# Optimization experiments

Hardware: AMD Instinct MI355X
Metric: run time of the kernel (lower is better)

## Reference

```python
import jax, jax.numpy as jnp
import numpy as np
import math

D_MODEL = 512
EXPAND = 2
D_INNER = EXPAND * D_MODEL          # 1024
HEADDIM = 8
NHEADS = D_INNER // HEADDIM         # 128
NGROUPS = 2
D_STATE = 16
CONV_DIM = D_INNER + 2 * NGROUPS * D_STATE   # 1088
D_IN_PROJ = 2 * D_INNER + 2 * NGROUPS * D_STATE + NHEADS  # 2240
P13 = [(0, 0), (1, 1)]
P31 = [(1, 1), (0, 0)]
P33 = [(1, 1), (1, 1)]


def silu(x):
    return x * jax.nn.sigmoid(x)


def dwconv(x, w, pad):
    # depthwise 2D conv; x: (B,C,H,W), w: (C,1,kh,kw)
    return jax.lax.conv_general_dilated(
        x, w, (1, 1), pad,
        dimension_numbers=('NCHW', 'OIHW', 'NCHW'),
        feature_group_count=x.shape[1])


def interleave_ch(a, b):
    # channel-interleave: out[:, ::2] = a, out[:, 1::2] = b
    Bn, C, Hh, Ww = a.shape
    return jnp.stack([a, b], axis=2).reshape(Bn, 2 * C, Hh, Ww)


def linear_attn(x, dt, A, Bm, Cm, Dp):
    # non-causal linear-attention duality of Mamba2 (grouped heads)
    # x: (B,L,h,p), dt: (B,L,h), A: (h,) negative, Bm/Cm: (B,L,g*ds), Dp: (h,)
    b, L, h, p = x.shape
    g, ds = NGROUPS, D_STATE
    dA = -(dt * A[None, None, :])          # ssd_positive_dA -> positive
    Vs = x * dA[..., None]
    K = Bm.reshape(b, L, g, ds)
    Q = Cm.reshape(b, L, g, ds)
    Vg = Vs.reshape(b, L, h // g, g, p)
    KV = jnp.einsum('blgs,blmgp->bmgsp', K, Vg)       # (b, h/g, g, ds, p)
    y = jnp.einsum('blgs,bmgsp->blmgp', Q, KV)        # (b, L, h/g, g, p)
    y = y + (x * Dp[None, None, :, None]).reshape(b, L, h // g, g, p)
    return y.reshape(b, L, h, p)


def setup_inputs() -> dict:
    key = jax.random.key(0)
    ks = jax.random.split(key, 20)
    Bn, Hh, Ww = 8, 64, 64
    L = Hh * Ww
    u = jax.random.normal(ks[0], (Bn, L, D_MODEL), jnp.float32)
    W_in = jax.random.normal(ks[1], (D_IN_PROJ, D_MODEL), jnp.float32) / math.sqrt(D_MODEL)
    dt = jnp.exp(jax.random.uniform(ks[2], (NHEADS,)) * (math.log(0.1) - math.log(0.001)) + math.log(0.001))
    dt = jnp.clip(dt, 1e-4, None)
    dt_bias = dt + jnp.log(-jnp.expm1(-dt))
    A_log = jnp.log(jax.random.uniform(ks[3], (NHEADS,), minval=1.0, maxval=16.0))
    Dp = jnp.ones((NHEADS,), jnp.float32)

    def cw(k, c, kh, kw):
        return jax.random.normal(k, (c, 1, kh, kw), jnp.float32) / math.sqrt(kh * kw)

    bcC = 2 * NGROUPS * D_STATE // 4  # 16
    w_conv2d = cw(ks[4], CONV_DIM // 2, 3, 3)
    w13x1 = cw(ks[5], D_INNER // 4, 1, 3)
    w31x1 = cw(ks[6], D_INNER // 4, 3, 1)
    w13x2 = cw(ks[7], D_INNER // 4, 1, 3)
    w31x2 = cw(ks[8], D_INNER // 4, 3, 1)
    w13bc1 = cw(ks[9], bcC, 1, 3)
    w31bc1 = cw(ks[10], bcC, 3, 1)
    w13bc2 = cw(ks[11], bcC, 1, 3)
    w31bc2 = cw(ks[12], bcC, 3, 1)
    w_conv2d_z = cw(ks[13], D_INNER, 3, 3)
    ln_g = jnp.ones((D_INNER,), jnp.float32)
    ln_b = jnp.zeros((D_INNER,), jnp.float32)
    scale = jnp.float32(1.0)
    shift = jnp.float32(0.0)
    alpha1 = jnp.float32(1.0)
    alpha2 = jnp.float32(1.0)
    W_out = jax.random.normal(ks[14], (D_MODEL, 2 * D_INNER), jnp.float32) / math.sqrt(2 * D_INNER)
    return dict(u=u, H=Hh, W=Ww, W_in=W_in, dt_bias=dt_bias, A_log=A_log, Dp=Dp,
                w_conv2d=w_conv2d, w13x1=w13x1, w31x1=w31x1, w13x2=w13x2, w31x2=w31x2,
                w13bc1=w13bc1, w31bc1=w31bc1, w13bc2=w13bc2, w31bc2=w31bc2,
                w_conv2d_z=w_conv2d_z, ln_g=ln_g, ln_b=ln_b, scale=scale, shift=shift,
                alpha1=alpha1, alpha2=alpha2, W_out=W_out)


def reference(u, H, W, W_in, dt_bias, A_log, Dp, w_conv2d, w13x1, w31x1, w13x2, w31x2,
              w13bc1, w31bc1, w13bc2, w31bc2, w_conv2d_z, ln_g, ln_b, scale, shift,
              alpha1, alpha2, W_out):
    Bn, L, _ = u.shape
    zxbcdt = u @ W_in.T                                 # (B,L,2240)
    z = zxbcdt[..., :D_INNER]
    xBC = zxbcdt[..., D_INNER:D_INNER + CONV_DIM]
    dt = zxbcdt[..., D_INNER + CONV_DIM:]
    dt = jax.nn.softplus(dt + dt_bias)                  # (B,L,h)

    # even/odd channel-interleave split, reshape to NCHW feature maps
    even = xBC[..., 0::2].reshape(Bn, H, W, -1).transpose(0, 3, 1, 2)
    odd = xBC[..., 1::2].reshape(Bn, H, W, -1).transpose(0, 3, 1, 2)
    even = silu(dwconv(even, w_conv2d, P33))

    oe = odd[:, 0::2]
    oo = odd[:, 1::2]
    x_oe, bc_oe = oe[:, :D_INNER // 4], oe[:, D_INNER // 4:]
    x_oo, bc_oo = oo[:, :D_INNER // 4], oo[:, D_INNER // 4:]
    x_oe = silu(dwconv(dwconv(x_oe, w31x1, P31), w13x1, P13))
    x_oo = silu(dwconv(dwconv(x_oo, w13x2, P13), w31x2, P31))
    bc_oe = silu(dwconv(dwconv(bc_oe, w13bc1, P13), w31bc1, P31))
    bc_oo = silu(dwconv(dwconv(bc_oo, w31bc2, P31), w13bc2, P13))
    xbc_oe = jnp.concatenate([x_oe, bc_oe], axis=1)
    xbc_oo = jnp.concatenate([x_oo, bc_oo], axis=1)
    odd = interleave_ch(xbc_oe, xbc_oo)

    xBCc = interleave_ch(even, odd)                     # (B, CONV_DIM, H, W)
    xBCc = xBCc.transpose(0, 2, 3, 1).reshape(Bn, L, CONV_DIM)
    x = xBCc[..., :D_INNER]
    Bm = xBCc[..., D_INNER:D_INNER + NGROUPS * D_STATE]
    Cm = xBCc[..., D_INNER + NGROUPS * D_STATE:]

    A = -jnp.exp(A_log)
    y = linear_attn(x.reshape(Bn, L, NHEADS, HEADDIM), dt, A, Bm, Cm, Dp)
    y = y.reshape(Bn, L, D_INNER)

    mu = y.mean(-1, keepdims=True)
    var = ((y - mu) ** 2).mean(-1, keepdims=True)
    y = (y - mu) / jnp.sqrt(var + 1e-5) * ln_g + ln_b
    y = y * scale + shift

    zc = z.reshape(Bn, H, W, D_INNER).transpose(0, 3, 1, 2)
    zc = silu(dwconv(zc, w_conv2d_z, P33))
    zc = zc.transpose(0, 2, 3, 1).reshape(Bn, L, D_INNER)

    out = jnp.concatenate([alpha1 * y, alpha2 * zc], axis=-1) @ W_out.T
    return out
```

## Files before the change

### kernel.cpp

```cpp
#include <hip/hip_runtime.h>
#include <hip/hip_bf16.h>
#include <cstdint>
#include <cstddef>

#define HDIM    64
#define WDIM    64
#define LPB     4096
#define DMODEL  512
#define DIN     1024
#define CONVD   1088
#define DPROJ   2240
#define NHEADS  128
#define NCV     2112

using f16    = _Float16;
using f16x4  = __attribute__((ext_vector_type(4))) _Float16;
using f16x8  = __attribute__((ext_vector_type(8))) _Float16;
using f32x4  = __attribute__((ext_vector_type(4))) float;

__device__ __forceinline__ float siluf(float x) { return x / (1.f + __expf(-x)); }
__device__ __forceinline__ float fsilu(float x) {
  return x * __builtin_amdgcn_rcpf(1.f + __expf(-x));
}

__device__ __forceinline__ void fma_mix_lo(float& acc, unsigned a, unsigned b) {
  asm("v_fma_mix_f32 %0, %1, %2, %0 op_sel_hi:[1,1,0]" : "+v"(acc) : "v"(a), "v"(b));
}
__device__ __forceinline__ void fma_mix_hi(float& acc, unsigned a, unsigned b) {
  asm("v_fma_mix_f32 %0, %1, %2, %0 op_sel:[1,1,0] op_sel_hi:[1,1,0]" : "+v"(acc) : "v"(a), "v"(b));
}
__device__ __forceinline__ void fmixl(float& acc, unsigned a, float b) {
  asm("v_fma_mix_f32 %0, %1, %2, %0 op_sel_hi:[1,0,0]" : "+v"(acc) : "v"(a), "v"(b));
}
__device__ __forceinline__ void fmixh(float& acc, unsigned a, float b) {
  asm("v_fma_mix_f32 %0, %1, %2, %0 op_sel:[1,0,0] op_sel_hi:[1,0,0]" : "+v"(acc) : "v"(a), "v"(b));
}

__device__ __forceinline__ void fma8(float* acc, const uint4& v, const uint4& w) {
  fma_mix_lo(acc[0], v.x, w.x);  fma_mix_hi(acc[1], v.x, w.x);
  fma_mix_lo(acc[2], v.y, w.y);  fma_mix_hi(acc[3], v.y, w.y);
  fma_mix_lo(acc[4], v.z, w.z);  fma_mix_hi(acc[5], v.z, w.z);
  fma_mix_lo(acc[6], v.w, w.w);  fma_mix_hi(acc[7], v.w, w.w);
}

__global__ __launch_bounds__(256) void k_cvt(const float* __restrict__ in, f16* __restrict__ out) {
  size_t i = ((size_t)blockIdx.x * 256 + threadIdx.x) * 4;
  f32x4 v = *(const f32x4*)(in + i);
  f16x4 o;
  #pragma unroll
  for (int j = 0; j < 4; ++j) o[j] = (f16)v[j];
  *(f16x4*)(out + i) = o;
}

__global__ __launch_bounds__(256) void k_cvt_win(const float* __restrict__ W, f16* __restrict__ out) {
  int i = blockIdx.x * 256 + threadIdx.x;
  int row = i >> 9, col = i & 511;
  float v = (row < DPROJ) ? W[row * 512 + col] : 0.f;
  out[i] = (f16)v;
}

__global__ __launch_bounds__(256) void k_keff(const float* __restrict__ w33,
                       const float* __restrict__ w13x1, const float* __restrict__ w31x1,
                       const float* __restrict__ w13x2, const float* __restrict__ w31x2,
                       const float* __restrict__ w13bc1, const float* __restrict__ w31bc1,
                       const float* __restrict__ w13bc2, const float* __restrict__ w31bc2,
                       const float* __restrict__ wz,
                       f16* __restrict__ keffall) {
  int j = blockIdx.x * 256 + threadIdx.x;
  if (j >= NCV) return;
  if (j < 1024) {
    #pragma unroll
    for (int tap = 0; tap < 9; ++tap) keffall[tap * NCV + j] = (f16)wz[j * 9 + tap];
    return;
  }
  int jj = j - 1024;
  float kh[3] = {0,0,0}, kw[3] = {0,0,0};
  bool dense = ((jj & 1) == 0);
  if (!dense) {
    int m = jj >> 2;
    if ((jj & 3) == 1) {
      if (m < 256) { for (int t=0;t<3;++t){ kh[t]=w31x1[m*3+t];  kw[t]=w13x1[m*3+t];  } }
      else { int q=m-256; for (int t=0;t<3;++t){ kh[t]=w31bc1[q*3+t]; kw[t]=w13bc1[q*3+t]; } }
    } else {
      if (m < 256) { for (int t=0;t<3;++t){ kh[t]=w31x2[m*3+t];  kw[t]=w13x2[m*3+t];  } }
      else { int q=m-256; for (int t=0;t<3;++t){ kh[t]=w31bc2[q*3+t]; kw[t]=w13bc2[q*3+t]; } }
    }
  }
  #pragma unroll
  for (int dh = 0; dh < 3; ++dh)
    #pragma unroll
    for (int dw = 0; dw < 3; ++dw) {
      float v = dense ? w33[(jj >> 1) * 9 + dh*3 + dw] : kh[dh] * kw[dw];
      keffall[(dh*3 + dw) * NCV + j] = (f16)v;
    }
}

template<typename OutT>
__global__ __launch_bounds__(256) void k_gemmf(const f16* __restrict__ A, int lda,
                                               const f16* __restrict__ Bm, int ldb,
                                               OutT* __restrict__ C, int ldc,
                                               int Kseg, int NW, int ntn, int ntmn, long Cseg) {
  __shared__ __align__(16) f16 As[128 * 32];
  __shared__ __align__(16) f16 Bs[128 * 32];

  int nwg = gridDim.x, bid = blockIdx.x;
  int q = nwg >> 3, r = nwg & 7;
  int xcd = bid & 7, loc = bid >> 3;
  int wg  = (xcd < r ? xcd * (q + 1) : r * (q + 1) + (xcd - r) * q) + loc;
  int kseg = wg / ntmn;
  int rem  = wg - kseg * ntmn;
  long m0 = (long)(rem / ntn) * 128;
  long n0 = (long)(rem % ntn) * 128;
  const int kbase = kseg * Kseg;

  const int tid  = threadIdx.x;
  const int w    = tid >> 6, lane = tid & 63;
  const int wr   = w >> 1, wc = w & 1;

  f32x4 acc[4][4];
  #pragma unroll
  for (int i = 0; i < 4; ++i)
    #pragma unroll
    for (int j = 0; j < 4; ++j) acc[i][j] = (f32x4){0.f,0.f,0.f,0.f};

  const int srow = w * 16 + (lane >> 2);
  const int scol = (lane & 3) * 8;
  const long aoff = (m0 + srow) * (long)lda + scol + kbase;
  const long boff = (n0 + srow) * (long)ldb + scol + kbase;
  const int fr = lane & 15;
  const int kc = (lane >> 4) * 8;

  for (int k0 = 0; k0 < Kseg; k0 += 32) {
    #pragma unroll
    for (int i = 0; i < 2; ++i) {
      long ao = aoff + (long)i*64*lda + k0;
      long bo = boff + (long)i*64*ldb + k0;
      int ls = (i*4 + w) * 512;
      __builtin_amdgcn_global_load_lds((const __attribute__((address_space(1))) void*)(A + ao),
                                       (__attribute__((address_space(3))) void*)&As[ls], 16, 0, 0);
      __builtin_amdgcn_global_load_lds((const __attribute__((address_space(1))) void*)(Bm + bo),
                                       (__attribute__((address_space(3))) void*)&Bs[ls], 16, 0, 0);
    }
    __syncthreads();
    f16x8 af[4], bf[4];
    #pragma unroll
    for (int f = 0; f < 4; ++f) {
      af[f] = *(const f16x8*)&As[(wr*64 + f*16 + fr) * 32 + kc];
      bf[f] = *(const f16x8*)&Bs[(wc*64 + f*16 + fr) * 32 + kc];
    }
    #pragma unroll
    for (int i = 0; i < 4; ++i)
      #pragma unroll
      for (int j = 0; j < 4; ++j)
        acc[i][j] = __builtin_amdgcn_mfma_f32_16x16x32_f16(af[i], bf[j], acc[i][j], 0, 0, 0);
    __syncthreads();
  }

  OutT* Cb = C + (long)kseg * Cseg;
  const int cr = (lane >> 4) * 4;
  const int cc = lane & 15;
  #pragma unroll
  for (int i = 0; i < 4; ++i) {
    long rbase = m0 + wr*64 + i*16 + cr;
    #pragma unroll
    for (int j = 0; j < 4; ++j) {
      int col = (int)n0 + wc*64 + j*16 + cc;
      if (col < NW) {
        OutT* cp = Cb + rbase * (long)ldc + col;
        #pragma unroll
        for (int r = 0; r < 4; ++r) cp[(long)r * ldc] = (OutT)acc[i][j][r];
      }
    }
  }
}

__global__ __launch_bounds__(256) void k_red2h(const f16* __restrict__ part, long seg,
                                               float* __restrict__ out) {
  long i = ((long)blockIdx.x * 256 + threadIdx.x) * 4;
  f16x4 s0 = *(const f16x4*)(part + i);
  f16x4 s1 = *(const f16x4*)(part + seg + i);
  f32x4 o;
  #pragma unroll
  for (int j = 0; j < 4; ++j) o[j] = (float)s0[j] + (float)s1[j];
  *(f32x4*)(out + i) = o;
}

__global__ __launch_bounds__(192) void k_conv_all(const f16* __restrict__ zx,
                                                  const f16* __restrict__ keffall,
                                                  const float* __restrict__ a2_p,
                                                  const float* __restrict__ dt_bias,
                                                  const float* __restrict__ A_log,
                                                  f16* __restrict__ xbc,
                                                  f16* __restrict__ g2,
                                                  float* __restrict__ dAb) {
  int t = threadIdx.x;
  int bid = blockIdx.x, qq = gridDim.x >> 3;
  int grp = (bid & 7) * qq + (bid >> 3);
  int l0 = grp * 2;
  long lb = (long)(l0 & ~(LPB - 1));
  int h  = (l0 >> 6) & 63;
  int w0 = l0 & 63;

  if (t < 132) {
    int c0 = t * 8;
    int c1 = c0 + 1056;
    float a00[8] = {0,0,0,0,0,0,0,0};
    float a01[8] = {0,0,0,0,0,0,0,0};
    float a10[8] = {0,0,0,0,0,0,0,0};
    float a11[8] = {0,0,0,0,0,0,0,0};
    const uint4 z4 = {0u,0u,0u,0u};

    #pragma unroll
    for (int dh = 0; dh < 3; ++dh) {
      int hh = h + dh - 1;
      if (hh < 0 || hh >= HDIM) continue;
      const f16* rp = zx + (lb + (long)(hh * 64)) * DPROJ;
      uint4 v0[4], v1[4];
      #pragma unroll
      for (int pp = 0; pp < 4; ++pp) {
        int ww = w0 + pp - 1;
        ww = ww < 0 ? 0 : (ww > 63 ? 63 : ww);
        const f16* tp = rp + (long)ww * DPROJ;
        v0[pp] = *(const uint4*)(tp + c0);
        v1[pp] = *(const uint4*)(tp + c1);
      }
      if (w0 == 0)  { v0[0] = z4; v1[0] = z4; }
      if (w0 == 62) { v0[3] = z4; v1[3] = z4; }
      #pragma unroll
      for (int dw = 0; dw < 3; ++dw) {
        uint4 wa = *(const uint4*)&keffall[(dh*3 + dw) * NCV + c0];
        uint4 wb = *(const uint4*)&keffall[(dh*3 + dw) * NCV + c1];
        fma8(a00, v0[dw],     wa);
        fma8(a10, v0[dw + 1], wa);
        fma8(a01, v1[dw],     wb);
        fma8(a11, v1[dw + 1], wb);
      }
    }

    float a2 = a2_p[0];
    #pragma unroll
    for (int ti = 0; ti < 2; ++ti) {
      long l = l0 + ti;
      const float* pc0 = ti ? a10 : a00;
      const float* pc1 = ti ? a11 : a01;
      f16x8 o8;
      if (c0 < 1024) {
        #pragma unroll
        for (int j = 0; j < 8; ++j) o8[j] = (f16)(a2 * fsilu(pc0[j]));
        *(f16x8*)&g2[l * 2048 + 1024 + c0] = o8;
      } else {
        #pragma unroll
        for (int j = 0; j < 8; ++j) o8[j] = (f16)fsilu(pc0[j]);
        *(f16x8*)&xbc[l * (long)CONVD + (c0 - 1024)] = o8;
      }
      f16x8 o9;
      #pragma unroll
      for (int j = 0; j < 8; ++j) o9[j] = (f16)fsilu(pc1[j]);
      *(f16x8*)&xbc[l * (long)CONVD + (c1 - 1024)] = o9;
    }
  } else if (t < 164) {
    int idx = t - 132;
    int ti = idx >> 4;
    int hd = (idx & 15) * 8;
    long l = l0 + ti;
    f16x8 x = *(const f16x8*)&zx[l * (long)DPROJ + NCV + hd];
    f32x4 o0, o1;
    #pragma unroll
    for (int j = 0; j < 8; ++j) {
      float xx = (float)x[j] + dt_bias[hd + j];
      float sp = (xx > 20.f) ? xx : log1pf(__expf(xx));
      float dv = sp * __expf(A_log[hd + j]);
      if (j < 4) o0[j] = dv; else o1[j-4] = dv;
    }
    *(f32x4*)&dAb[l * 128 + hd]     = o0;
    *(f32x4*)&dAb[l * 128 + hd + 4] = o1;
  }
}

__global__ __launch_bounds__(512) void k_kv_part(const f16* __restrict__ xbc,
                                                 const float* __restrict__ dA,
                                                 float* __restrict__ part) {
  int t = threadIdx.x;
  int m = t >> 3, p = t & 7;
  int lc = blockIdx.x, b = blockIdx.y;
  float acc0[16], acc1[16];
  #pragma unroll
  for (int s = 0; s < 16; ++s) { acc0[s] = 0.f; acc1[s] = 0.f; }
  long lbase = (long)b * LPB + lc * 32;
  #pragma unroll 2
  for (int li = 0; li < 32; ++li) {
    long row = lbase + li;
    const f16* xr = xbc + row * CONVD;
    float2 aa = *(const float2*)&dA[row * 128 + 2*m];
    float xv0 = (float)xr[16*m + p]     * aa.x;
    float xv1 = (float)xr[16*m + 8 + p] * aa.y;
    uint4 q0 = *(const uint4*)(xr + DIN);
    uint4 q1 = *(const uint4*)(xr + DIN + 8);
    uint4 q2 = *(const uint4*)(xr + DIN + 16);
    uint4 q3 = *(const uint4*)(xr + DIN + 24);
    unsigned a0[4] = {q0.x, q0.y, q0.z, q0.w};
    unsigned a1[4] = {q1.x, q1.y, q1.z, q1.w};
    unsigned a2v[4] = {q2.x, q2.y, q2.z, q2.w};
    unsigned a3[4] = {q3.x, q3.y, q3.z, q3.w};
    #pragma unroll
    for (int k = 0; k < 4; ++k) {
      fmixl(acc0[2*k],     a0[k], xv0);  fmixh(acc0[2*k+1],     a0[k], xv0);
      fmixl(acc0[8+2*k],   a1[k], xv0);  fmixh(acc0[8+2*k+1],   a1[k], xv0);
      fmixl(acc1[2*k],     a2v[k], xv1); fmixh(acc1[2*k+1],     a2v[k], xv1);
      fmixl(acc1[8+2*k],   a3[k], xv1);  fmixh(acc1[8+2*k+1],   a3[k], xv1);
    }
  }
  long base = ((long)(b*128 + lc)) * 16384 + (long)m * 256;
  #pragma unroll
  for (int s = 0; s < 16; ++s) {
    part[base + s*8 + p]       = acc0[s];
    part[base + 128 + s*8 + p] = acc1[s];
  }
}

__global__ __launch_bounds__(256) void k_kv_red(const float* __restrict__ part,
                                                float* __restrict__ KV) {
  int e = blockIdx.x * 256 + threadIdx.x;
  int b = blockIdx.y;
  float s = 0.f;
  #pragma unroll 4
  for (int lc = 0; lc < 128; ++lc) s += part[((long)(b*128 + lc)) * 16384 + e];
  KV[(long)b * 16384 + e] = s;
}

__global__ __launch_bounds__(256) void k_y_ln(const f16* __restrict__ xbc,
                                              const float* __restrict__ KV,
                                              const float* __restrict__ Dp,
                                              const float* __restrict__ ln_g,
                                              const float* __restrict__ ln_b,
                                              const float* __restrict__ sc_p,
                                              const float* __restrict__ sh_p,
                                              const float* __restrict__ a1_p,
                                              f16* __restrict__ g2) {
  __shared__ float Qs[32][32];
  __shared__ float red[2][8];
  int t = threadIdx.x;
  int hd = t >> 1, pb = (t & 1) * 4;
  int m = hd >> 1, g = hd & 1;
  int b = blockIdx.x >> 7;
  long l0 = (long)b * LPB + (blockIdx.x & 127) * 32;

  f32x4 kv[16];
  #pragma unroll
  for (int s = 0; s < 16; ++s)
    kv[s] = *(const f32x4*)&KV[(long)b * 16384 + m*256 + g*128 + s*8 + pb];

  if (t < 128) {
    int tok = t >> 2, q8 = (t & 3) * 8;
    f16x8 qv = *(const f16x8*)&xbc[(l0 + tok) * CONVD + 1056 + q8];
    #pragma unroll
    for (int j = 0; j < 8; ++j) Qs[tok][q8 + j] = (float)qv[j];
  }
  int c0 = hd*8 + pb;
  f32x4 lg = *(const f32x4*)&ln_g[c0];
  f32x4 lb = *(const f32x4*)&ln_b[c0];
  float dpv = Dp[hd];
  float sc = sc_p[0], sh = sh_p[0], a1 = a1_p[0];
  int wv = t >> 6, lane = t & 63;
  __syncthreads();

  for (int tok = 0; tok < 32; ++tok) {
    long row = l0 + tok;
    f16x4 xr4 = *(const f16x4*)&xbc[row * CONVD + c0];
    f32x4 yv;
    #pragma unroll
    for (int j = 0; j < 4; ++j) yv[j] = (float)xr4[j] * dpv;
    #pragma unroll
    for (int s = 0; s < 16; ++s) {
      float qv = Qs[tok][g*16 + s];
      #pragma unroll
      for (int j = 0; j < 4; ++j) yv[j] = fmaf(qv, kv[s][j], yv[j]);
    }
    float s1 = yv[0] + yv[1] + yv[2] + yv[3];
    float s2 = yv[0]*yv[0] + yv[1]*yv[1] + yv[2]*yv[2] + yv[3]*yv[3];
    #pragma unroll
    for (int off = 1; off < 64; off <<= 1) {
      s1 += __shfl_xor(s1, off, 64);
      s2 += __shfl_xor(s2, off, 64);
    }
    if (lane == 0) { red[tok & 1][wv*2] = s1; red[tok & 1][wv*2 + 1] = s2; }
    __syncthreads();
    const float* rr = red[tok & 1];
    float S1 = rr[0] + rr[2] + rr[4] + rr[6];
    float S2 = rr[1] + rr[3] + rr[5] + rr[7];
    float mu   = S1 * (1.f/1024.f);
    float var  = S2 * (1.f/1024.f) - mu*mu;
    float rstd = rsqrtf(var + 1e-5f);
    f16x4 o4;
    #pragma unroll
    for (int j = 0; j < 4; ++j) {
      float yn = (yv[j] - mu) * rstd * lg[j] + lb[j];
      o4[j] = (f16)(a1 * (yn * sc + sh));
    }
    *(f16x4*)&g2[row * 2048 + c0] = o4;
  }
}

extern "C" void kernel_launch(void* const* d_in, const int* in_sizes, int n_in,
                              void* d_out, int out_size, void* d_ws, size_t ws_size,
                              hipStream_t stream) {
  const float* u       = (const float*)d_in[0];
  const float* W_in    = (const float*)d_in[3];
  const float* dt_bias = (const float*)d_in[4];
  const float* A_log   = (const float*)d_in[5];
  const float* Dp      = (const float*)d_in[6];
  const float* w33     = (const float*)d_in[7];
  const float* w13x1   = (const float*)d_in[8];
  const float* w31x1   = (const float*)d_in[9];
  const float* w13x2   = (const float*)d_in[10];
  const float* w31x2   = (const float*)d_in[11];
  const float* w13bc1  = (const float*)d_in[12];
  const float* w31bc1  = (const float*)d_in[13];
  const float* w13bc2  = (const float*)d_in[14];
  const float* w31bc2  = (const float*)d_in[15];
  const float* wz      = (const float*)d_in[16];
  const float* ln_g    = (const float*)d_in[17];
  const float* ln_b    = (const float*)d_in[18];
  const float* sc      = (const float*)d_in[19];
  const float* sh      = (const float*)d_in[20];
  const float* a1      = (const float*)d_in[21];
  const float* a2      = (const float*)d_in[22];
  const float* W_out   = (const float*)d_in[23];

  const size_t B_G2   = 16777216;
  const size_t B_ZX   = 18350080;
  const size_t B_XBC  = 8912896;
  const size_t B_DA   = 2097152;
  const size_t B_KV   = 65536;
  const size_t perC   = B_G2 + B_ZX + B_XBC + B_DA + B_KV;
  const size_t persist = 2359296 + 2097152 + 38912;

  int C = 8;
  while (C > 1 && persist + (size_t)C * perC > ws_size) C >>= 1;
  const int nch = 8 / C;
  const int Mc  = C * LPB;

  char* p = (char*)d_ws;
  f16*   win_f   = (f16*)p;   p += 2359296;
  f16*   wout_f  = (f16*)p;   p += 2097152;
  f16*   keffall = (f16*)p;   p += 38912;
  char*  arena   = p;
  f16*   g2      = (f16*)arena;
  f16*   u_f     = (f16*)arena;
  p = arena + (size_t)C * B_G2;
  f16*   zx      = (f16*)p;   p += (size_t)C * B_ZX;
  f16*   xbc     = (f16*)p;   p += (size_t)C * B_XBC;
  float* dAb     = (float*)p; p += (size_t)C * B_DA;
  float* KV      = (float*)p; p += (size_t)C * B_KV;
  float* part   = (float*)zx;
  f16*   kpart  = (f16*)zx;

  k_cvt_win<<<4608, 256, 0, stream>>>(W_in, win_f);
  k_cvt    <<<1024, 256, 0, stream>>>(W_out, wout_f);
  k_keff   <<<9, 256, 0, stream>>>(w33, w13x1, w31x1, w13x2, w31x2,
                                   w13bc1, w31bc1, w13bc2, w31bc2, wz, keffall);

  for (int ch = 0; ch < nch; ++ch) {
    const float* uc   = u + (size_t)ch * Mc * 512;
    float*       outc = (float*)d_out + (size_t)ch * Mc * 512;
    const int ntm = Mc / 128;

    k_cvt<<<Mc/2, 256, 0, stream>>>(uc, u_f);

    k_gemmf<f16><<<ntm*18, 256, 0, stream>>>(u_f, 512, win_f, 512,
                                             zx, DPROJ, 512, DPROJ, 18, ntm*18, 0);

    k_conv_all<<<Mc/2, 192, 0, stream>>>(zx, keffall, a2, dt_bias, A_log,
                                         xbc, g2, dAb);

    k_kv_part <<<dim3(128, C), 512, 0, stream>>>(xbc, dAb, part);
    k_kv_red  <<<dim3(64, C), 256, 0, stream>>>(part, KV);
    k_y_ln    <<<C*128, 256, 0, stream>>>(xbc, KV, Dp, ln_g, ln_b, sc, sh, a1, g2);

    const long cseg = (long)Mc * 512;
    k_gemmf<f16><<<ntm*4*2, 256, 0, stream>>>(g2, 2048, wout_f, 2048,
                                              kpart, 512, 1024, 512, 4, ntm*4, cseg);
    k_red2h<<<Mc/2, 256, 0, stream>>>(kpart, cseg, outc);
  }
}
```

Measured before the change: 539.7 us.

## Use 256x256-tile double-buffered GEMM with direct-to-LDS loads for input projection

Adds a new GEMM kernel for the input projection with 256x256 output tiles, 512 threads and one workgroup per CU. It double-buffers 64-wide K slices in LDS using global_load_lds, with XOR swizzling and staged vmcnt waits so the next tile's loads overlap the current tile's MFMAs. The larger tile is meant to raise data reuse and cut global traffic, and the explicit pipeline aims to hide memory latency. In exchange it uses far more registers and LDS, launches fewer workgroups, and relies on hand-counted waitcnts for correctness.

```diff
diff --git a/kernel.cpp b/kernel.cpp
--- a/kernel.cpp
+++ b/kernel.cpp
@@ -18,6 +18,9 @@
 using f16x8  = __attribute__((ext_vector_type(8))) _Float16;
 using f32x4  = __attribute__((ext_vector_type(4))) float;
 
+#define VM_CNT(n) asm volatile("s_waitcnt vmcnt(" #n ")" ::: "memory")
+#define LDSFENCE  asm volatile("" ::: "memory")
+
 __device__ __forceinline__ float siluf(float x) { return x / (1.f + __expf(-x)); }
 __device__ __forceinline__ float fsilu(float x) {
   return x * __builtin_amdgcn_rcpf(1.f + __expf(-x));
@@ -35,7 +38,6 @@
 __device__ __forceinline__ void fmixh(float& acc, unsigned a, float b) {
   asm("v_fma_mix_f32 %0, %1, %2, %0 op_sel:[1,0,0] op_sel_hi:[1,0,0]" : "+v"(acc) : "v"(a), "v"(b));
 }
-
 __device__ __forceinline__ void fma8(float* acc, const uint4& v, const uint4& w) {
   fma_mix_lo(acc[0], v.x, w.x);  fma_mix_hi(acc[1], v.x, w.x);
   fma_mix_lo(acc[2], v.y, w.y);  fma_mix_hi(acc[3], v.y, w.y);
@@ -95,6 +97,133 @@
     }
 }
 
+__global__ __launch_bounds__(512, 1) void k_gemm8(const f16* __restrict__ A, int lda,
+                                                  const f16* __restrict__ Bm, int ldb,
+                                                  f16* __restrict__ C, int ldc,
+                                                  int K, int NW, int ntn) {
+  __shared__ __align__(16) f16 Al[2 * 16384];
+  __shared__ __align__(16) f16 Bl[2 * 16384];
+
+  int nwg = gridDim.x, bid = blockIdx.x;
+  int q = nwg >> 3, r = nwg & 7;
+  int xcd = bid & 7, loc = bid >> 3;
+  int wg  = (xcd < r ? xcd * (q + 1) : r * (q + 1) + (xcd - r) * q) + loc;
+  long m0 = (long)(wg / ntn) * 256;
+  long n0 = (long)(wg % ntn) * 256;
+
+  const int tid  = threadIdx.x;
+  const int wid  = tid >> 6, lane = tid & 63;
+  const int wr   = wid >> 2, wc = wid & 3;
+
+  const int rowoff = wid * 8 + (lane >> 3);
+  const int scolS  = ((lane & 7) ^ (lane >> 3)) * 8;
+  const int ldst   = wid * 512;
+
+  const int fr   = lane & 15;
+  const int koff = (lane >> 4) * 8;
+  const int swz8 = (lane & 7) << 3;
+
+  f32x4 acc[8][4];
+  #pragma unroll
+  for (int i = 0; i < 8; ++i)
+    #pragma unroll
+    for (int j = 0; j < 4; ++j) acc[i][j] = (f32x4){0.f,0.f,0.f,0.f};
+
+  const int NT = K >> 6;
+
+  auto stA = [&](int par, int X, int kb) {
+    __builtin_amdgcn_global_load_lds(
+      (const __attribute__((address_space(1))) void*)(A + (m0 + X*64 + rowoff) * (long)lda + kb + scolS),
+      (__attribute__((address_space(3))) void*)&Al[par*16384 + X*4096 + ldst], 16, 0, 0);
+  };
+  auto stB = [&](int par, int X, int kb) {
+    __builtin_amdgcn_global_load_lds(
+      (const __attribute__((address_space(1))) void*)(Bm + (n0 + X*64 + rowoff) * (long)ldb + kb + scolS),
+      (__attribute__((address_space(3))) void*)&Bl[par*16384 + X*4096 + ldst], 16, 0, 0);
+  };
+
+  stB(0,0,0); stB(0,1,0); stB(0,2,0); stB(0,3,0);
+  stA(0,0,0); stA(0,2,0); stA(0,1,0); stA(0,3,0);
+
+  for (int t = 0; t < NT; ++t) {
+    const bool last = (t == NT - 1);
+    const int pr = t & 1, pw = (t + 1) & 1;
+    const int kb = (t + 1) << 6;
+    const f16* Ard = &Al[pr * 16384];
+    const f16* Brd = &Bl[pr * 16384];
+    f16x8 bf[4][2];
+
+    #pragma unroll
+    for (int s = 0; s < 4; ++s) {
+      f16x8 af[2][2];
+      if (s == 1 || s == 3) {
+        #pragma unroll
+        for (int j = 0; j < 2; ++j)
+          #pragma unroll
+          for (int k = 0; k < 2; ++k) {
+            int rr = wr*128 + (2*s + j)*16 + fr;
+            af[j][k] = *(const f16x8*)&Ard[rr*64 + ((k*32 + koff) ^ swz8)];
+          }
+      }
+      if (!last) {
+        if (s == 0)      { stB(pw, 0, kb); stB(pw, 1, kb); }
+        else if (s == 1) { stB(pw, 2, kb); stB(pw, 3, kb); }
+        else if (s == 2) { stA(pw, 0, kb); stA(pw, 2, kb); }
+        else             { stA(pw, 1, kb); stA(pw, 3, kb); }
+      }
+      if (s == 0) { if (!last) { VM_CNT(4); } else { VM_CNT(2); } }
+      if (s == 2) { if (!last) { VM_CNT(6); } else { VM_CNT(0); } }
+      __builtin_amdgcn_s_barrier();
+      LDSFENCE;
+      if (s == 0) {
+        #pragma unroll
+        for (int ni = 0; ni < 4; ++ni)
+          #pragma unroll
+          for (int k = 0; k < 2; ++k) {
+            int rr = wc*64 + ni*16 + fr;
+            bf[ni][k] = *(const f16x8*)&Brd[rr*64 + ((k*32 + koff) ^ swz8)];
+          }
+      }
+      if (s == 0 || s == 2) {
+        #pragma unroll
+        for (int j = 0; j < 2; ++j)
+          #pragma unroll
+          for (int k = 0; k < 2; ++k) {
+            int rr = wr*128 + (2*s + j)*16 + fr;
+            af[j][k] = *(const f16x8*)&Ard[rr*64 + ((k*32 + koff) ^ swz8)];
+          }
+      }
+      __builtin_amdgcn_s_setprio(1);
+      #pragma unroll
+      for (int j = 0; j < 2; ++j)
+        #pragma unroll
+        for (int ni = 0; ni < 4; ++ni)
+          #pragma unroll
+          for (int k = 0; k < 2; ++k)
+            acc[2*s + j][ni] = __builtin_amdgcn_mfma_f32_16x16x32_f16(af[j][k], bf[ni][k], acc[2*s + j][ni], 0, 0, 0);
+      __builtin_amdgcn_s_setprio(0);
+      __builtin_amdgcn_s_barrier();
+      LDSFENCE;
+    }
+  }
+
+  const int cr = (lane >> 4) * 4;
+  const int cc = lane & 15;
+  #pragma unroll
+  for (int mi = 0; mi < 8; ++mi) {
+    long rbase = m0 + wr*128 + mi*16 + cr;
+    #pragma unroll
+    for (int ni = 0; ni < 4; ++ni) {
+      int col = (int)n0 + wc*64 + ni*16 + cc;
+      if (col < NW) {
+        f16* cp = C + rbase * (long)ldc + col;
+        #pragma unroll
+        for (int rr2 = 0; rr2 < 4; ++rr2) cp[(long)rr2 * ldc] = (f16)acc[mi][ni][rr2];
+      }
+    }
+  }
+}
+
 template<typename OutT>
 __global__ __launch_bounds__(256) void k_gemmf(const f16* __restrict__ A, int lda,
                                                const f16* __restrict__ Bm, int ldb,
@@ -168,7 +297,7 @@
       if (col < NW) {
         OutT* cp = Cb + rbase * (long)ldc + col;
         #pragma unroll
-        for (int r = 0; r < 4; ++r) cp[(long)r * ldc] = (OutT)acc[i][j][r];
+        for (int r2 = 0; r2 < 4; ++r2) cp[(long)r2 * ldc] = (OutT)acc[i][j][r2];
       }
     }
   }
@@ -467,8 +596,8 @@
 
     k_cvt<<<Mc/2, 256, 0, stream>>>(uc, u_f);
 
-    k_gemmf<f16><<<ntm*18, 256, 0, stream>>>(u_f, 512, win_f, 512,
-                                             zx, DPROJ, 512, DPROJ, 18, ntm*18, 0);
+    k_gemm8<<<(Mc/256)*9, 512, 0, stream>>>(u_f, 512, win_f, 512,
+                                            zx, DPROJ, 512, DPROJ, 9);
 
     k_conv_all<<<Mc/2, 192, 0, stream>>>(zx, keffall, a2, dt_bias, A_log,
                                          xbc, g2, dAb);
```

After: 544.3 us. No clear change (+0.9%).
